# Optimization experiments

Hardware: AMD Instinct MI355X
Metric: run time of the kernel (lower is better)

## Reference

```python
import jax, jax.numpy as jnp
import numpy as np
import math

D_MODEL = 128

def setup_inputs() -> dict:
    key = jax.random.key(0)
    k1, k2, k3, k4 = jax.random.split(key, 4)
    B, V, F = 8, 32, 512
    x = jax.random.normal(k1, (B, V, F), dtype=jnp.float32)
    # Dense(d_model) on a scalar input: kernel shape [1, d_model], no bias
    w_q = jax.random.normal(k2, (1, D_MODEL), dtype=jnp.float32)
    w_k = jax.random.normal(k3, (1, D_MODEL), dtype=jnp.float32)
    w_v = jax.random.normal(k4, (1, D_MODEL), dtype=jnp.float32)
    return {"x": x, "w_q": w_q, "w_k": w_k, "w_v": w_v}

def reference(x, w_q, w_k, w_v):
    d_model = w_q.shape[-1]
    # x: [B, V, F]; per-scalar projections -> [B, V, F, d_model]
    Q = x[..., None] * w_q[0]  # broadcast outer product
    K = x[..., None] * w_k[0]
    V = x[..., None] * w_v[0]
    # scores: [B, V, F, F]
    scores = jnp.einsum('bvfd,bvgd->bvfg', Q, K) / math.sqrt(d_model)
    attn = jax.nn.softmax(scores, axis=-1)
    attended = jnp.einsum('bvfg,bvgd->bvfd', attn, V)
    # mean over the n_filters axis -> [B, V, d_model]
    return attended.mean(axis=2)
```

## Files before the change

kernel.cpp:

```cpp
#include <hip/hip_runtime.h>
#include <math.h>


#if __has_builtin(__builtin_amdgcn_exp2f)
#define EXP2(x) __builtin_amdgcn_exp2f(x)
#else
#define EXP2(x) exp2f(x)
#endif

typedef float v2f __attribute__((ext_vector_type(2)));

#define F_DIM 512

__global__ __launch_bounds__(1024) void intravol_attn(
    const float* __restrict__ x,
    const float* __restrict__ wq,
    const float* __restrict__ wk,
    const float* __restrict__ wv,
    float* __restrict__ out)
{
    __shared__ __align__(16) float xs[F_DIM];
    __shared__ __align__(8) float pden[4][F_DIM];
    __shared__ __align__(8) float pnum[4][F_DIM];
    __shared__ float wmax[8], wmin[8], wsum[8];
    __shared__ float s_c, s_xmax, s_xmin;

    const int tid  = threadIdx.x;
    const int lane = tid & 63;
    const int wave = tid >> 6;
    const int row  = blockIdx.x;

    float xv = 0.0f;
    if (tid < F_DIM) { xv = x[row * F_DIM + tid]; xs[tid] = xv; }
    if (wave < 8) {
        float mx = xv, mn = xv;
        for (int o = 32; o > 0; o >>= 1) {
            mx = fmaxf(mx, __shfl_down(mx, o));
            mn = fminf(mn, __shfl_down(mn, o));
        }
        if (lane == 0) { wmax[wave] = mx; wmin[wave] = mn; }
    } else if (wave == 8) {
        float d = wq[lane] * wk[lane] + wq[lane + 64] * wk[lane + 64];
        for (int o = 32; o > 0; o >>= 1) d += __shfl_down(d, o);
        if (lane == 0) s_c = d * 0.08838834764831845f;
    }
    __syncthreads();
    if (tid == 0) {
        float M = wmax[0], m_ = wmin[0];
        #pragma unroll
        for (int i = 1; i < 8; ++i) { M = fmaxf(M, wmax[i]); m_ = fminf(m_, wmin[i]); }
        s_xmax = M; s_xmin = m_;
    }
    __syncthreads();

    const float LOG2E = 1.4426950408889634f;
    const int f0 = (tid & 255) << 1;
    const int sl = tid >> 8;

    const float a0 = s_c * xs[f0]     * LOG2E;
    const float a1 = s_c * xs[f0 + 1] * LOG2E;
    v2f a2  = { a0, a1 };
    v2f bb  = { -((a0 >= 0.0f) ? a0 * s_xmax : a0 * s_xmin),
                -((a1 >= 0.0f) ? a1 * s_xmax : a1 * s_xmin) };
    v2f den = { 0.0f, 0.0f };
    v2f num = { 0.0f, 0.0f };

    const float4* xs4 = (const float4*)&xs[sl << 7];
    #pragma unroll 8
    for (int i = 0; i < 32; ++i) {
        const float4 v = xs4[i];
        const float xg_[4] = { v.x, v.y, v.z, v.w };
        #pragma unroll
        for (int j = 0; j < 4; ++j) {
            const float xg = xg_[j];
            const v2f xg2 = { xg, xg };
            const v2f arg = __builtin_elementwise_fma(a2, xg2, bb);
            const v2f e   = { EXP2(arg.x), EXP2(arg.y) };
            den += e;
            num = __builtin_elementwise_fma(e, xg2, num);
        }
    }
    *(v2f*)&pden[sl][f0] = den;
    *(v2f*)&pnum[sl][f0] = num;
    __syncthreads();

    float sf = 0.0f;
    if (tid < F_DIM) {
        float D = 0.0f, N = 0.0f;
        #pragma unroll
        for (int s = 0; s < 4; ++s) { D += pden[s][tid]; N += pnum[s][tid]; }
        sf = N / D;
    }
    float t = sf;
    for (int o = 32; o > 0; o >>= 1) t += __shfl_down(t, o);
    if (lane == 0 && wave < 8) wsum[wave] = t;
    __syncthreads();

    if (tid < 128) {
        float total = 0.0f;
        #pragma unroll
        for (int i = 0; i < 8; ++i) total += wsum[i];
        out[row * 128 + tid] = total * (1.0f / (float)F_DIM) * wv[tid];
    }
}

extern "C" void kernel_launch(void* const* d_in, const int* in_sizes, int n_in,
                              void* d_out, int out_size, void* d_ws, size_t ws_size,
                              hipStream_t stream) {
    const float* x  = (const float*)d_in[0];
    const float* wq = (const float*)d_in[1];
    const float* wk = (const float*)d_in[2];
    const float* wv = (const float*)d_in[3];
    float* out = (float*)d_out;

    intravol_attn<<<256, 1024, 0, stream>>>(x, wq, wk, wv, out);
}
```

Baseline: 67.34 us.

## Replace pairwise softmax exponentials with a moment-based Taylor expansion fast path

Since scores are rank-1 (c·x_f·x_g), the kernel now computes power moments of the normalized row values in shared memory. It then evaluates the softmax numerator and denominator for each query as a truncated 64-term Taylor series in c·x_f, replacing the O(F²) exp loop with O(F·terms) work. A per-row guard based on the value range and c chooses between this path and the original exact exp2 loop. The trade-off is reduced accuracy from truncation and float cancellation when the exponent range is large. The kernel also needs a large shared-memory pool of about 70KB per block.

```diff
diff --git a/kernel.cpp b/kernel.cpp
--- a/kernel.cpp
+++ b/kernel.cpp
@@ -11,6 +11,8 @@
 typedef float v2f __attribute__((ext_vector_type(2)));
 
 #define F_DIM 512
+#define NTERM 64
+#define ROWW 34
 
 __global__ __launch_bounds__(1024) void intravol_attn(
     const float* __restrict__ x,
@@ -19,11 +21,13 @@
     const float* __restrict__ wv,
     float* __restrict__ out)
 {
+    __shared__ __align__(16) float pool[F_DIM * ROWW];
     __shared__ __align__(16) float xs[F_DIM];
-    __shared__ __align__(8) float pden[4][F_DIM];
-    __shared__ __align__(8) float pnum[4][F_DIM];
+    __shared__ v2f   pm2[33][17];
+    __shared__ float mom[NTERM + 2];
     __shared__ float wmax[8], wmin[8], wsum[8];
-    __shared__ float s_c, s_xmax, s_xmin;
+    __shared__ float s_c, s_xmax, s_xmin, s_scale, s_inv;
+    __shared__ int   s_fast;
 
     const int tid  = threadIdx.x;
     const int lane = tid & 63;
@@ -50,47 +54,143 @@
         #pragma unroll
         for (int i = 1; i < 8; ++i) { M = fmaxf(M, wmax[i]); m_ = fminf(m_, wmin[i]); }
         s_xmax = M; s_xmin = m_;
+        const float ap = fmaxf(M, 0.0f), an = fmaxf(-m_, 0.0f);
+        const float xa = fmaxf(fmaxf(ap, an), 1e-30f);
+        const float tm = fabsf(s_c) * xa * xa;
+        const float ms = fminf(ap, an) / xa;
+        s_scale = xa;
+        s_inv   = 1.0f / xa;
+        s_fast = (tm <= 26.0f) && (tm * (1.0f - ms) <= 3.0f) ? 1 : 0;
     }
     __syncthreads();
 
-    const float LOG2E = 1.4426950408889634f;
-    const int f0 = (tid & 255) << 1;
-    const int sl = tid >> 8;
-
-    const float a0 = s_c * xs[f0]     * LOG2E;
-    const float a1 = s_c * xs[f0 + 1] * LOG2E;
-    v2f a2  = { a0, a1 };
-    v2f bb  = { -((a0 >= 0.0f) ? a0 * s_xmax : a0 * s_xmin),
-                -((a1 >= 0.0f) ? a1 * s_xmax : a1 * s_xmin) };
-    v2f den = { 0.0f, 0.0f };
-    v2f num = { 0.0f, 0.0f };
-
-    const float4* xs4 = (const float4*)&xs[sl << 7];
-    #pragma unroll 8
-    for (int i = 0; i < 32; ++i) {
-        const float4 v = xs4[i];
-        const float xg_[4] = { v.x, v.y, v.z, v.w };
-        #pragma unroll
-        for (int j = 0; j < 4; ++j) {
-            const float xg = xg_[j];
-            const v2f xg2 = { xg, xg };
-            const v2f arg = __builtin_elementwise_fma(a2, xg2, bb);
-            const v2f e   = { EXP2(arg.x), EXP2(arg.y) };
-            den += e;
-            num = __builtin_elementwise_fma(e, xg2, num);
-        }
-    }
-    *(v2f*)&pden[sl][f0] = den;
-    *(v2f*)&pnum[sl][f0] = num;
-    __syncthreads();
-
     float sf = 0.0f;
-    if (tid < F_DIM) {
-        float D = 0.0f, N = 0.0f;
-        #pragma unroll
-        for (int s = 0; s < 4; ++s) { D += pden[s][tid]; N += pnum[s][tid]; }
-        sf = N / D;
-    }
+
+    if (s_fast) {
+        if (tid < F_DIM) {
+            const float u  = xv * s_inv;
+            const float w  = u * u;
+            const float w2 = w * w;
+            v2f* rowp = (v2f*)&pool[tid * ROWW];
+            v2f first; first.x = u; first.y = w;
+            rowp[0] = first;
+            v2f pr;  pr.x = w2; pr.y = w2 * w;
+            v2f ww;  ww.x = w2; ww.y = w2;
+            #pragma unroll
+            for (int m = 1; m <= 16; ++m) {
+                rowp[m] = pr;
+                pr *= ww;
+            }
+        }
+        __syncthreads();
+
+        if (lane <= 32) {
+            const float* rowbase = &pool[(wave << 5) * ROWW];
+            float sw = 0.0f, su = 0.0f;
+            #pragma unroll
+            for (int j = 0; j < 32; ++j) {
+                const float rp = rowbase[j * ROWW + lane];
+                const float ru = rowbase[j * ROWW];
+                sw += rp;
+                su  = fmaf(rp, ru, su);
+            }
+            v2f t; t.x = sw; t.y = su;
+            pm2[lane][wave] = t;
+        }
+        __syncthreads();
+        if (tid < 33) {
+            v2f s; s.x = 0.0f; s.y = 0.0f;
+            #pragma unroll
+            for (int c = 0; c < 16; ++c) s += pm2[tid][c];
+            if (tid == 0) {
+                mom[0] = (float)F_DIM;
+                mom[1] = s.x;  mom[2] = s.y;
+            } else {
+                mom[2 * tid]     = s.x;
+                mom[2 * tid + 1] = s.y;
+            }
+        }
+        __syncthreads();
+
+        {
+            const int f   = tid & 511;
+            const int par = tid >> 9;
+            const float tau = s_c * xs[f] * s_scale;
+            const float r2  = tau * tau;
+            float den = 0.0f, num = 0.0f;
+            if (par == 0) {
+                float p = 1.0f;
+                #pragma unroll
+                for (int j = 0; j < 32; ++j) {
+                    const int n = 2 * j;
+                    den = fmaf(mom[n],     p, den);
+                    num = fmaf(mom[n + 1], p, num);
+                    p *= (1.0f / (float)((n + 1) * (n + 2)));
+                    p *= r2;
+                }
+            } else {
+                float p = tau;
+                #pragma unroll
+                for (int j = 0; j < 32; ++j) {
+                    const int n = 2 * j + 1;
+                    den = fmaf(mom[n],     p, den);
+                    num = fmaf(mom[n + 1], p, num);
+                    p *= (1.0f / (float)((n + 1) * (n + 2)));
+                    p *= r2;
+                }
+            }
+            v2f a; a.x = den; a.y = num;
+            ((v2f*)pool)[tid] = a;
+        }
+        __syncthreads();
+        if (tid < F_DIM) {
+            const v2f a = ((v2f*)pool)[tid];
+            const v2f b = ((v2f*)pool)[tid + 512];
+            sf = s_scale * (a.y + b.y) / (a.x + b.x);
+        }
+    } else {
+        float (*pden)[F_DIM] = (float (*)[F_DIM])pool;
+        float (*pnum)[F_DIM] = (float (*)[F_DIM])(pool + 4 * F_DIM);
+
+        const float LOG2E = 1.4426950408889634f;
+        const int f0 = (tid & 255) << 1;
+        const int sl = tid >> 8;
+
+        const float a0 = s_c * xs[f0]     * LOG2E;
+        const float a1 = s_c * xs[f0 + 1] * LOG2E;
+        v2f a2  = { a0, a1 };
+        v2f bb  = { -((a0 >= 0.0f) ? a0 * s_xmax : a0 * s_xmin),
+                    -((a1 >= 0.0f) ? a1 * s_xmax : a1 * s_xmin) };
+        v2f den = { 0.0f, 0.0f };
+        v2f num = { 0.0f, 0.0f };
+
+        const float4* xs4 = (const float4*)&xs[sl << 7];
+        #pragma unroll 8
+        for (int i = 0; i < 32; ++i) {
+            const float4 v = xs4[i];
+            const float xg_[4] = { v.x, v.y, v.z, v.w };
+            #pragma unroll
+            for (int j = 0; j < 4; ++j) {
+                const float xg = xg_[j];
+                const v2f xg2 = { xg, xg };
+                const v2f arg = __builtin_elementwise_fma(a2, xg2, bb);
+                const v2f e   = { EXP2(arg.x), EXP2(arg.y) };
+                den += e;
+                num = __builtin_elementwise_fma(e, xg2, num);
+            }
+        }
+        *(v2f*)&pden[sl][f0] = den;
+        *(v2f*)&pnum[sl][f0] = num;
+        __syncthreads();
+
+        if (tid < F_DIM) {
+            float D = 0.0f, N = 0.0f;
+            #pragma unroll
+            for (int s = 0; s < 4; ++s) { D += pden[s][tid]; N += pnum[s][tid]; }
+            sf = N / D;
+        }
+    }
+
     float t = sf;
     for (int o = 32; o > 0; o >>= 1) t += __shfl_down(t, o);
     if (lane == 0 && wave < 8) wsum[wave] = t;
```

After: 62.22 us. 1.08x faster.

## Replace pairwise exp softmax with a guarded Taylor moment expansion

Applied to the files above, without the earlier changes.

Adds a fast path that expands exp(c*x_f*x_g) as a power series in x_g. It precomputes power rows of the normalised x in shared memory, reduces them into moments with wave reductions, and evaluates the numerator and denominator per query as polynomials in c*x_f. This turns the O(F^2) exponential work into roughly O(F*32) multiply-adds. The path is only taken when a per-row check on the range of c*x^2 says the truncated series is accurate; otherwise the original exp loop runs. The cost is a much larger shared-memory buffer and an extra reduction stage, and accuracy depends on the truncation bound.

```diff
diff --git a/kernel.cpp b/kernel.cpp
--- a/kernel.cpp
+++ b/kernel.cpp
@@ -9,6 +9,7 @@
 #endif
 
 typedef float v2f __attribute__((ext_vector_type(2)));
+typedef float v4f __attribute__((ext_vector_type(4)));
 
 #define F_DIM 512
 
@@ -19,11 +20,12 @@
     const float* __restrict__ wv,
     float* __restrict__ out)
 {
+    __shared__ __align__(16) float pool[33 * F_DIM];
     __shared__ __align__(16) float xs[F_DIM];
-    __shared__ __align__(8) float pden[4][F_DIM];
-    __shared__ __align__(8) float pnum[4][F_DIM];
-    __shared__ float wmax[8], wmin[8], wsum[8];
-    __shared__ float s_c, s_xmax, s_xmin;
+    __shared__ __align__(16) float mpack[2][64];
+    __shared__ float wmax[8], wmin[8], wsum[16];
+    __shared__ float s_c, s_xmax, s_xmin, s_scale, s_inv;
+    __shared__ int   s_fast;
 
     const int tid  = threadIdx.x;
     const int lane = tid & 63;
@@ -50,57 +52,158 @@
         #pragma unroll
         for (int i = 1; i < 8; ++i) { M = fmaxf(M, wmax[i]); m_ = fminf(m_, wmin[i]); }
         s_xmax = M; s_xmin = m_;
+        const float ap = fmaxf(M, 0.0f), an = fmaxf(-m_, 0.0f);
+        const float xa = fmaxf(fmaxf(ap, an), 1e-30f);
+        const float tm = fabsf(s_c) * xa * xa;
+        const float ms = fminf(ap, an) / xa;
+        s_scale = xa;
+        s_inv   = 1.0f / xa;
+        s_fast = (tm <= 26.0f) && (tm * (1.0f - ms) <= 3.0f) ? 1 : 0;
+        mpack[0][0] = (float)F_DIM;
     }
     __syncthreads();
 
-    const float LOG2E = 1.4426950408889634f;
-    const int f0 = (tid & 255) << 1;
-    const int sl = tid >> 8;
-
-    const float a0 = s_c * xs[f0]     * LOG2E;
-    const float a1 = s_c * xs[f0 + 1] * LOG2E;
-    v2f a2  = { a0, a1 };
-    v2f bb  = { -((a0 >= 0.0f) ? a0 * s_xmax : a0 * s_xmin),
-                -((a1 >= 0.0f) ? a1 * s_xmax : a1 * s_xmin) };
-    v2f den = { 0.0f, 0.0f };
-    v2f num = { 0.0f, 0.0f };
-
-    const float4* xs4 = (const float4*)&xs[sl << 7];
-    #pragma unroll 8
-    for (int i = 0; i < 32; ++i) {
-        const float4 v = xs4[i];
-        const float xg_[4] = { v.x, v.y, v.z, v.w };
-        #pragma unroll
-        for (int j = 0; j < 4; ++j) {
-            const float xg = xg_[j];
-            const v2f xg2 = { xg, xg };
-            const v2f arg = __builtin_elementwise_fma(a2, xg2, bb);
-            const v2f e   = { EXP2(arg.x), EXP2(arg.y) };
-            den += e;
-            num = __builtin_elementwise_fma(e, xg2, num);
-        }
-    }
-    *(v2f*)&pden[sl][f0] = den;
-    *(v2f*)&pnum[sl][f0] = num;
-    __syncthreads();
-
     float sf = 0.0f;
-    if (tid < F_DIM) {
-        float D = 0.0f, N = 0.0f;
-        #pragma unroll
-        for (int s = 0; s < 4; ++s) { D += pden[s][tid]; N += pnum[s][tid]; }
-        sf = N / D;
-    }
+
+    if (s_fast) {
+        {
+            const int g = tid & 511;
+            if (tid < F_DIM) {
+                const float u = xv * s_inv;
+                const float w = u * u;
+                pool[g] = u;
+                float p = w;
+                #pragma unroll
+                for (int k = 1; k <= 16; ++k) { pool[k * F_DIM + g] = p; p *= w; }
+            } else {
+                const float u  = xs[g] * s_inv;
+                const float w  = u * u;
+                const float w2 = w * w, w4 = w2 * w2, w8 = w4 * w4;
+                float p = w8 * w8 * w;
+                #pragma unroll
+                for (int k = 17; k <= 32; ++k) { pool[k * F_DIM + g] = p; p *= w; }
+            }
+        }
+        __syncthreads();
+
+        {
+            const v4f* ubp = (const v4f*)pool;
+            const v4f ua = ubp[lane];
+            const v4f uc = ubp[64 + lane];
+
+            auto do_row = [&](int k) {
+                const v4f* rb = (const v4f*)&pool[k * F_DIM];
+                const v4f pa = rb[lane];
+                const v4f pb = rb[64 + lane];
+                float sA = ((pa.x + pa.y) + (pa.z + pa.w)) +
+                           ((pb.x + pb.y) + (pb.z + pb.w));
+                float sB = fmaf(ua.x, pa.x, fmaf(ua.y, pa.y,
+                           fmaf(ua.z, pa.z, fmaf(ua.w, pa.w,
+                           fmaf(uc.x, pb.x, fmaf(uc.y, pb.y,
+                           fmaf(uc.z, pb.z, uc.w * pb.w)))))));
+                #pragma unroll
+                for (int o = 32; o > 0; o >>= 1) {
+                    sA += __shfl_down(sA, o);
+                    sB += __shfl_down(sB, o);
+                }
+                if (lane == 0) {
+                    if (k == 0) {
+                        mpack[0][1] = sA;
+                        mpack[1][0] = sA;
+                    } else {
+                        if (k < 32) {
+                            mpack[0][2 * k]     = sA;
+                            mpack[0][2 * k + 1] = sB;
+                            mpack[1][2 * k]     = sB / (float)(2 * k + 1);
+                        }
+                        mpack[1][2 * k - 1]     = sA / (float)(2 * k - 1);
+                    }
+                }
+            };
+            do_row(wave);
+            do_row(wave + 16);
+            if (wave == 0) do_row(32);
+        }
+        __syncthreads();
+
+        {
+            const int par = lane & 1;
+            const int f   = (wave << 5) | (lane >> 1);
+            const float tau = s_c * xs[f] * s_scale;
+            const float r2  = tau * tau;
+            float p   = par ? tau : 1.0f;
+            float den = 0.0f, num = 0.0f;
+            const v4f* mp = (const v4f*)&mpack[par][0];
+            #pragma unroll
+            for (int t = 0; t < 16; ++t) {
+                const v4f m = mp[t];
+                den = fmaf(m.x, p, den);
+                num = fmaf(m.y, p, num);
+                p *= r2;
+                p *= (1.0f / (float)((4 * t + 1) * (4 * t + 2)));
+                den = fmaf(m.z, p, den);
+                num = fmaf(m.w, p, num);
+                p *= r2;
+                p *= (1.0f / (float)((4 * t + 3) * (4 * t + 4)));
+            }
+            den += __shfl_xor(den, 1);
+            num += __shfl_xor(num, 1);
+            sf = s_scale * num / den;
+        }
+    } else {
+        float (*pden)[F_DIM] = (float (*)[F_DIM])pool;
+        float (*pnum)[F_DIM] = (float (*)[F_DIM])(pool + 4 * F_DIM);
+
+        const float LOG2E = 1.4426950408889634f;
+        const int f0 = (tid & 255) << 1;
+        const int sl = tid >> 8;
+
+        const float a0 = s_c * xs[f0]     * LOG2E;
+        const float a1 = s_c * xs[f0 + 1] * LOG2E;
+        v2f a2  = { a0, a1 };
+        v2f bb  = { -((a0 >= 0.0f) ? a0 * s_xmax : a0 * s_xmin),
+                    -((a1 >= 0.0f) ? a1 * s_xmax : a1 * s_xmin) };
+        v2f den = { 0.0f, 0.0f };
+        v2f num = { 0.0f, 0.0f };
+
+        const float4* xs4 = (const float4*)&xs[sl << 7];
+        #pragma unroll 8
+        for (int i = 0; i < 32; ++i) {
+            const float4 v = xs4[i];
+            const float xg_[4] = { v.x, v.y, v.z, v.w };
+            #pragma unroll
+            for (int j = 0; j < 4; ++j) {
+                const float xg = xg_[j];
+                const v2f xg2 = { xg, xg };
+                const v2f arg = __builtin_elementwise_fma(a2, xg2, bb);
+                const v2f e   = { EXP2(arg.x), EXP2(arg.y) };
+                den += e;
+                num = __builtin_elementwise_fma(e, xg2, num);
+            }
+        }
+        *(v2f*)&pden[sl][f0] = den;
+        *(v2f*)&pnum[sl][f0] = num;
+        __syncthreads();
+
+        if (tid < F_DIM) {
+            float D = 0.0f, N = 0.0f;
+            #pragma unroll
+            for (int s = 0; s < 4; ++s) { D += pden[s][tid]; N += pnum[s][tid]; }
+            sf = N / D;
+        }
+    }
+
     float t = sf;
     for (int o = 32; o > 0; o >>= 1) t += __shfl_down(t, o);
-    if (lane == 0 && wave < 8) wsum[wave] = t;
+    if (lane == 0) wsum[wave] = t;
     __syncthreads();
 
     if (tid < 128) {
+        const float esc = s_fast ? (1.0f / 1024.0f) : (1.0f / 512.0f);
         float total = 0.0f;
         #pragma unroll
-        for (int i = 0; i < 8; ++i) total += wsum[i];
-        out[row * 128 + tid] = total * (1.0f / (float)F_DIM) * wv[tid];
+        for (int i = 0; i < 16; ++i) total += wsum[i];
+        out[row * 128 + tid] = total * esc * wv[tid];
     }
 }
 
```

New measurement: 62.56 us. -7.1%, faster.
